# Performance work log

Measured on AMD Instinct MI355X. Metric: run time of the kernel, lower is better.

The kernel has to match this reference:

```python
import jax, jax.numpy as jnp
import numpy as np

B, S, D, H = 4, 1024, 1024, 16
DEPTH = D // H


def setup_inputs() -> dict:
    key = jax.random.key(0)
    ks = jax.random.split(key, 13)
    inp = {
        'query': jax.random.normal(ks[0], (B, S, D), dtype=jnp.float32),
        'key': jax.random.normal(ks[1], (B, S, D), dtype=jnp.float32),
        'value': jax.random.normal(ks[2], (B, S, D), dtype=jnp.float32),
        'mask': jax.random.bernoulli(ks[3], 0.1, (B, S, S)),
    }
    scale = 1.0 / np.sqrt(D)
    inp['wq_w'] = jax.random.uniform(ks[4], (D, D), jnp.float32, -scale, scale)
    inp['wq_b'] = jax.random.uniform(ks[5], (D,), jnp.float32, -scale, scale)
    inp['wk_w'] = jax.random.uniform(ks[6], (D, D), jnp.float32, -scale, scale)
    inp['wk_b'] = jax.random.uniform(ks[7], (D,), jnp.float32, -scale, scale)
    inp['wv_w'] = jax.random.uniform(ks[8], (D, D), jnp.float32, -scale, scale)
    inp['wv_b'] = jax.random.uniform(ks[9], (D,), jnp.float32, -scale, scale)
    inp['fc_w'] = jax.random.uniform(ks[10], (D, D), jnp.float32, -scale, scale)
    inp['fc_b'] = jax.random.uniform(ks[11], (D,), jnp.float32, -scale, scale)
    return inp


def _split_heads(x):
    # [B,S,D] -> [B,H,S,depth]
    b, s, _ = x.shape
    return x.reshape(b, s, H, DEPTH).transpose(0, 2, 1, 3)


def reference(query, key, value, mask, wq_w, wq_b, wk_w, wk_b, wv_w, wv_b, fc_w, fc_b):
    q = _split_heads(query @ wq_w.T + wq_b)
    k = _split_heads(key @ wk_w.T + wk_b)
    v = _split_heads(value @ wv_w.T + wv_b)
    scores = jnp.einsum('bhqd,bhkd->bhqk', q, k) / jnp.sqrt(jnp.float32(DEPTH))
    scores = jnp.where(mask[:, None, :, :], jnp.float32(-1e9), scores)
    attn = jax.nn.softmax(scores, axis=-1)
    out = jnp.einsum('bhqk,bhkd->bhqd', attn, v)  # [B,H,S,depth]
    out = out.transpose(0, 2, 1, 3).reshape(query.shape[0], -1, D)
    return out @ fc_w.T + fc_b
```

## Files before the change

kernel.cpp:

```cpp
#include <hip/hip_runtime.h>
#include <hip/hip_bf16.h>


typedef __bf16 bf16x8 __attribute__((ext_vector_type(8)));
typedef __bf16 bf16x4 __attribute__((ext_vector_type(4)));
typedef float  f32x4  __attribute__((ext_vector_type(4)));
typedef float  f32x16 __attribute__((ext_vector_type(16)));

typedef const __attribute__((address_space(1))) void* gptr_t;
typedef __attribute__((address_space(3))) void* lptr_t;

#define MFMA16(a, b, c) __builtin_amdgcn_mfma_f32_16x16x32_bf16((a), (b), (c), 0, 0, 0)
#define MFMA32(a, b, c) __builtin_amdgcn_mfma_f32_32x32x16_bf16((a), (b), (c), 0, 0, 0)

__device__ __forceinline__ void gload_lds16(const void* g, void* l) {
  __builtin_amdgcn_global_load_lds((gptr_t)g, (lptr_t)l, 16, 0, 0);
}

__device__ __forceinline__ unsigned pack2(float a, float b) {
  union { __bf16 h[2]; unsigned u; } x;
  x.h[0] = (__bf16)a; x.h[1] = (__bf16)b; return x.u;
}

__device__ __forceinline__ bf16x8 mkfrag(unsigned a, unsigned b, unsigned c, unsigned d) {
  union { unsigned w[4]; bf16x8 v; } x;
  x.w[0] = a; x.w[1] = b; x.w[2] = c; x.w[3] = d; return x.v;
}

__global__ void detect_mask(const unsigned char* m, int* flag) {
  __shared__ int s1[4], s23[4];
  int tid = threadIdx.x;
  uint4 v = ((const uint4*)m)[tid];
  unsigned x0 = v.x, x1 = v.y, x2 = v.z, x3 = v.w;
  unsigned c1  = (x0 & 0x0000ff00u) | (x1 & 0x0000ff00u) | (x2 & 0x0000ff00u) | (x3 & 0x0000ff00u);
  unsigned c23 = (x0 & 0xffff0000u) | (x1 & 0xffff0000u) | (x2 & 0xffff0000u) | (x3 & 0xffff0000u);
  unsigned long long b1 = __ballot(c1 != 0), b23 = __ballot(c23 != 0);
  if ((tid & 63) == 0) { s1[tid >> 6] = (b1 != 0); s23[tid >> 6] = (b23 != 0); }
  __syncthreads();
  if (tid == 0) {
    int a1 = s1[0] | s1[1] | s1[2] | s1[3];
    int a23 = s23[0] | s23[1] | s23[2] | s23[3];
    *flag = a1 ? 1 : (a23 ? 2 : 0);
  }
}

__global__ void pack_mask(const void* m, const int* flag, unsigned int* out) {
  size_t i = (size_t)blockIdx.x * 256 + threadIdx.x;
  int f = *flag;
  bool v;
  if (f == 1)      v = ((const unsigned char*)m)[i] != 0;
  else if (f == 2) v = ((const float*)m)[i] != 0.0f;
  else             v = ((const int*)m)[i] != 0;
  unsigned long long bal = __ballot(v);
  int lane = threadIdx.x & 63;
  if ((lane & 31) == 0) out[i >> 5] = (unsigned int)(bal >> (lane & 32));
}

__global__ void cvt_all(const float* q, const float* k, const float* v,
                        const float* w0, const float* w1, const float* w2, const float* w3,
                        __bf16* oq, __bf16* ok, __bf16* ov,
                        __bf16* o0, __bf16* o1, __bf16* o2, __bf16* o3) {
  int bid = blockIdx.x;
  const float* in; __bf16* out; int sub;
  if (bid < 12288) {
    int w = bid >> 12; sub = bid & 4095;
    in = w == 0 ? q : w == 1 ? k : v;
    out = w == 0 ? oq : w == 1 ? ok : ov;
  } else {
    int w = (bid - 12288) >> 10; sub = (bid - 12288) & 1023;
    in = w == 0 ? w0 : w == 1 ? w1 : w == 2 ? w2 : w3;
    out = w == 0 ? o0 : w == 1 ? o1 : w == 2 ? o2 : o3;
  }
  size_t i = (size_t)sub * 256 + threadIdx.x;
  float4 vv = ((const float4*)in)[i];
  bf16x4 o; o[0] = (__bf16)vv.x; o[1] = (__bf16)vv.y; o[2] = (__bf16)vv.z; o[3] = (__bf16)vv.w;
  ((bf16x4*)out)[i] = o;
}

__global__ __launch_bounds__(512, 2)
void gemm_qkv8(const __bf16* __restrict__ qb, const __bf16* __restrict__ kb,
               const __bf16* __restrict__ vb,
               const __bf16* __restrict__ wq, const __bf16* __restrict__ wk,
               const __bf16* __restrict__ wv,
               const float* __restrict__ bq, const float* __restrict__ bk,
               const float* __restrict__ bv,
               __bf16* __restrict__ Qp, __bf16* __restrict__ Kp, __bf16* __restrict__ Vt) {
  __shared__ __bf16 As[2][256 * 64];
  __shared__ __bf16 Bs[2][256 * 64];
  const int bm = blockIdx.x;
  const int bnall = blockIdx.y;
  const int which = bnall >> 2;
  const int bnl = bnall & 3;
  const __bf16* A = which == 0 ? qb : which == 1 ? kb : vb;
  const __bf16* W = which == 0 ? wq : which == 1 ? wk : wv;
  const float* bias = which == 0 ? bq : which == 1 ? bk : bv;

  const int tid = threadIdx.x, wave = tid >> 6, lane = tid & 63;
  const int wr = wave >> 2, wc = wave & 3;
  const int l15 = lane & 15, l4 = lane >> 4;
  const int srow = tid >> 3;
  const int sgw = ((tid & 7) ^ (srow & 7)) << 3;
  f32x4 acc[8][4] = {};

#define STAGE_HALF(bb, u, hp)                                                   \
  {                                                                             \
    _Pragma("unroll")                                                           \
    for (int i_ = 0; i_ < 2; ++i_) {                                            \
      int row_ = ((hp) & 1) * 128 + i_ * 64 + srow;                             \
      if ((hp) < 2)                                                             \
        gload_lds16(A + (size_t)(bm * 256 + row_) * 1024 + (u) * 64 + sgw,      \
                    &As[bb][(((hp) & 1) * 128 + i_ * 64 + wave * 8) * 64]);     \
      else                                                                      \
        gload_lds16(W + (size_t)(bnl * 256 + row_) * 1024 + (u) * 64 + sgw,     \
                    &Bs[bb][(((hp) & 1) * 128 + i_ * 64 + wave * 8) * 64]);     \
    }                                                                           \
  }

#define PHASE(curb, mh, nh, DOSTAGE)                                            \
  {                                                                             \
    bf16x8 af_[4][2], bf_[2][2];                                                \
    _Pragma("unroll")                                                           \
    for (int j_ = 0; j_ < 4; ++j_) {                                            \
      int row_ = wr * 128 + ((mh) * 4 + j_) * 16 + l15;                         \
      _Pragma("unroll")                                                         \
      for (int k_ = 0; k_ < 2; ++k_)                                            \
        af_[j_][k_] = *(const bf16x8*)(&As[curb][row_ * 64 +                    \
                          (((k_ * 4 + l4) ^ (row_ & 7)) << 3)]);                \
    }                                                                           \
    _Pragma("unroll")                                                           \
    for (int n_ = 0; n_ < 2; ++n_) {                                            \
      int row_ = wc * 64 + ((nh) * 2 + n_) * 16 + l15;                          \
      _Pragma("unroll")                                                         \
      for (int k_ = 0; k_ < 2; ++k_)                                            \
        bf_[n_][k_] = *(const bf16x8*)(&Bs[curb][row_ * 64 +                    \
                          (((k_ * 4 + l4) ^ (row_ & 7)) << 3)]);                \
    }                                                                           \
    DOSTAGE;                                                                    \
    __builtin_amdgcn_s_barrier();                                               \
    __builtin_amdgcn_sched_barrier(0);                                          \
    __builtin_amdgcn_s_setprio(1);                                              \
    _Pragma("unroll")                                                           \
    for (int k_ = 0; k_ < 2; ++k_)                                              \
      _Pragma("unroll")                                                         \
      for (int j_ = 0; j_ < 4; ++j_)                                            \
        _Pragma("unroll")                                                       \
        for (int n_ = 0; n_ < 2; ++n_)                                          \
          acc[(mh) * 4 + j_][(nh) * 2 + n_] =                                   \
              MFMA16(af_[j_][k_], bf_[n_][k_], acc[(mh) * 4 + j_][(nh) * 2 + n_]); \
    __builtin_amdgcn_s_setprio(0);                                              \
    __builtin_amdgcn_s_barrier();                                               \
    __builtin_amdgcn_sched_barrier(0);                                          \
  }

  STAGE_HALF(0, 0, 0); STAGE_HALF(0, 0, 1); STAGE_HALF(0, 0, 2); STAGE_HALF(0, 0, 3);
  int cur = 0;
#pragma unroll 1
  for (int u = 0; u < 16; ++u) {
    const int nu = u < 15 ? u + 1 : 15;
    const int oth = cur ^ 1;
    STAGE_HALF(oth, nu, 0);
    asm volatile("s_waitcnt vmcnt(2)" ::: "memory");
    __builtin_amdgcn_s_barrier();
    __builtin_amdgcn_sched_barrier(0);
    PHASE(cur, 0, 0, {});
    PHASE(cur, 1, 0, STAGE_HALF(oth, nu, 1));
    PHASE(cur, 0, 1, STAGE_HALF(oth, nu, 2));
    PHASE(cur, 1, 1, STAGE_HALF(oth, nu, 3));
    cur ^= 1;
  }

  const int r0 = l4 * 4, cl = l15;
  const float osc = (which == 0) ? 0.18033688011112042f : 1.0f;
  __bf16* Onat = which == 0 ? Qp : Kp;
#pragma unroll
  for (int ni = 0; ni < 4; ++ni) {
    int col = bnl * 256 + wc * 64 + ni * 16 + cl;
    float bvv = bias[col];
#pragma unroll
    for (int mi = 0; mi < 8; ++mi) {
      int rowb = bm * 256 + wr * 128 + mi * 16 + r0;
      if (which < 2) {
#pragma unroll
        for (int r = 0; r < 4; ++r)
          Onat[(size_t)(rowb + r) * 1024 + col] = (__bf16)((acc[mi][ni][r] + bvv) * osc);
      } else {
        int bb = rowb >> 10, s0 = rowb & 1023, hh = col >> 6, d = col & 63;
        bf16x4 ov;
#pragma unroll
        for (int r = 0; r < 4; ++r) ov[r] = (__bf16)(acc[mi][ni][r] + bvv);
        *(bf16x4*)(Vt + (((size_t)(bb * 16 + hh) * 64 + d) << 10) + s0) = ov;
      }
    }
  }
#undef STAGE_HALF
#undef PHASE
}

__global__ __launch_bounds__(256, 2)
void gemm_fc(const __bf16* __restrict__ A, const __bf16* __restrict__ W,
             const float* __restrict__ bias, float* __restrict__ C) {
  __shared__ __bf16 As[2][128 * 64];
  __shared__ __bf16 Bs[2][128 * 64];
  const int bm = blockIdx.x, bn = blockIdx.y;
  const int tid = threadIdx.x, wave = tid >> 6, lane = tid & 63;
  const int wr = wave >> 1, wc = wave & 1;
  const int rl = lane >> 3, c8 = lane & 7;
  f32x4 acc[4][4] = {};

#define FC_STAGE(bb, kt)                                                              \
  {                                                                                   \
    _Pragma("unroll")                                                                 \
    for (int i = 0; i < 4; ++i) {                                                     \
      int row = wave * 32 + i * 8 + rl;                                               \
      int sw = (c8 ^ (row & 7)) << 3;                                                 \
      gload_lds16(A + (size_t)(bm * 128 + row) * 1024 + (kt) * 64 + sw,               \
                  &As[bb][(wave * 32 + i * 8) * 64]);                                 \
      gload_lds16(W + (size_t)(bn * 128 + row) * 1024 + (kt) * 64 + sw,               \
                  &Bs[bb][(wave * 32 + i * 8) * 64]);                                 \
    }                                                                                 \
  }

  FC_STAGE(0, 0);
  __syncthreads();
  int buf = 0;
  for (int kt = 0; kt < 16; ++kt) {
    if (kt < 15) FC_STAGE(buf ^ 1, kt + 1);
#pragma unroll
    for (int k32 = 0; k32 < 2; ++k32) {
      bf16x8 af[4], bfr[4];
#pragma unroll
      for (int mi = 0; mi < 4; ++mi) {
        int row = wr * 64 + mi * 16 + (lane & 15);
        af[mi] = *(const bf16x8*)(&As[buf][row * 64 + (((k32 * 4 + (lane >> 4)) ^ (row & 7)) << 3)]);
      }
#pragma unroll
      for (int ni = 0; ni < 4; ++ni) {
        int row = wc * 64 + ni * 16 + (lane & 15);
        bfr[ni] = *(const bf16x8*)(&Bs[buf][row * 64 + (((k32 * 4 + (lane >> 4)) ^ (row & 7)) << 3)]);
      }
#pragma unroll
      for (int mi = 0; mi < 4; ++mi)
#pragma unroll
        for (int ni = 0; ni < 4; ++ni)
          acc[mi][ni] = MFMA16(af[mi], bfr[ni], acc[mi][ni]);
    }
    __syncthreads();
    buf ^= 1;
  }
  const int r0 = (lane >> 4) * 4, cl = lane & 15;
#pragma unroll
  for (int ni = 0; ni < 4; ++ni) {
    int col = bn * 128 + wc * 64 + ni * 16 + cl;
    float bvv = bias[col];
#pragma unroll
    for (int mi = 0; mi < 4; ++mi) {
      int rowb = bm * 128 + wr * 64 + mi * 16 + r0;
#pragma unroll
      for (int r = 0; r < 4; ++r)
        C[(size_t)(rowb + r) * 1024 + col] = acc[mi][ni][r] + bvv;
    }
  }
}

__global__ __launch_bounds__(256)
void attn32(const __bf16* __restrict__ Qp, const __bf16* __restrict__ Kp,
            const __bf16* __restrict__ Vt, const unsigned int* __restrict__ mp,
            __bf16* __restrict__ O) {
  __shared__ __bf16 Ks[2][64 * 64];
  __shared__ __bf16 Vs[2][64 * 64];
  const int tid = threadIdx.x, wave = tid >> 6, lane = tid & 63;
  const int lo5 = lane & 31, hi = lane >> 5;
  const int bx = blockIdx.x;
  const int qt = bx & 7, h = (bx >> 3) & 15, b = bx >> 7;
  const int qrow = qt * 128 + wave * 32 + lo5;

  const int srow = tid >> 3;
  const int sgx = ((tid & 7) ^ (srow & 7)) << 3;

#define ATTN_STAGE(bb, kt)                                                            \
  {                                                                                   \
    _Pragma("unroll")                                                                 \
    for (int i = 0; i < 2; ++i) {                                                     \
      gload_lds16(Kp + (size_t)(b * 1024 + (kt) * 64 + i * 32 + srow) * 1024          \
                     + h * 64 + sgx,                                                  \
                  &Ks[bb][i * 2048 + wave * 512]);                                    \
      gload_lds16(Vt + (size_t)((b * 16 + h) * 64 + i * 32 + srow) * 1024             \
                     + (kt) * 64 + sgx,                                               \
                  &Vs[bb][i * 2048 + wave * 512]);                                    \
    }                                                                                 \
  }

  bf16x8 qf[4];
  const __bf16* qb = Qp + ((size_t)(b * 1024 + qrow)) * 1024 + h * 64 + hi * 8;
#pragma unroll
  for (int m = 0; m < 4; ++m) qf[m] = *(const bf16x8*)(qb + m * 16);

  bf16x8 onesf;
#pragma unroll
  for (int i = 0; i < 8; ++i) onesf[i] = (__bf16)1.0f;

  f32x16 oacc0 = {}, oacc1 = {}, oaccD = {};
  const uint2* mrow = ((const uint2*)mp) + ((size_t)(b * 1024 + qrow)) * 16;
  const int x = lo5 & 7;

  ATTN_STAGE(0, 0);
  uint2 mwc = mrow[0];
  __syncthreads();
  int buf = 0;
  for (int kt = 0; kt < 16; ++kt) {
    if (kt < 15) ATTN_STAGE(buf ^ 1, kt + 1);
    uint2 mwn = mwc;
    if (kt < 15) mwn = mrow[kt + 1];
#pragma unroll
    for (int sub = 0; sub < 2; ++sub) {
      f32x16 s = {};
#pragma unroll
      for (int m = 0; m < 4; ++m) {
        bf16x8 kf = *(const bf16x8*)(&Ks[buf][(sub * 32 + lo5) * 64 + (((2 * m + hi) ^ x) << 3)]);
        s = MFMA32(kf, qf[m], s);
      }
      unsigned w32 = sub == 0 ? mwc.x : mwc.y;
      unsigned nw = ~(w32 >> (hi * 4));
      float p[16];
#pragma unroll
      for (int r = 0; r < 16; ++r) {
        float e = __builtin_amdgcn_exp2f(s[r]);
        unsigned keep = (unsigned)__builtin_amdgcn_sbfe((int)nw, (unsigned)((r & 3) + 8 * (r >> 2)), 1u);
        p[r] = __uint_as_float(__float_as_uint(e) & keep);
      }
      unsigned own[8];
#pragma unroll
      for (int u = 0; u < 4; ++u) {
        own[2 * u]     = pack2(p[4 * u],     p[4 * u + 1]);
        own[2 * u + 1] = pack2(p[4 * u + 2], p[4 * u + 3]);
      }
#pragma unroll
      for (int sf = 0; sf < 2; ++sf) {
        unsigned a0 = own[4 * sf + 0], b0 = own[4 * sf + 2];
        unsigned a1 = own[4 * sf + 1], b1 = own[4 * sf + 3];
        asm volatile("v_permlane32_swap_b32 %0, %1" : "+v"(a0), "+v"(b0));
        asm volatile("v_permlane32_swap_b32 %0, %1" : "+v"(a1), "+v"(b1));
        bf16x8 pa = mkfrag(a0, a1, b0, b1);
        int g = ((sub * 4 + sf * 2 + hi) ^ x) << 3;
        bf16x8 vf0 = *(const bf16x8*)(&Vs[buf][lo5 * 64 + g]);
        bf16x8 vf1 = *(const bf16x8*)(&Vs[buf][(lo5 + 32) * 64 + g]);
        oacc0 = MFMA32(pa, vf0, oacc0);
        oacc1 = MFMA32(pa, vf1, oacc1);
        oaccD = MFMA32(pa, onesf, oaccD);
      }
    }
    __syncthreads();
    buf ^= 1;
    mwc = mwn;
  }

  const size_t orow0 = (size_t)(b * 1024 + qt * 128 + wave * 32);
#pragma unroll
  for (int r = 0; r < 16; ++r) {
    int cr = (r & 3) + 8 * (r >> 2) + 4 * hi;
    float iv = __builtin_amdgcn_rcpf(oaccD[r]);
    __bf16* op = O + (orow0 + cr) * 1024 + h * 64 + lo5;
    op[0]  = (__bf16)(oacc0[r] * iv);
    op[32] = (__bf16)(oacc1[r] * iv);
  }
}

extern "C" void kernel_launch(void* const* d_in, const int* in_sizes, int n_in,
                              void* d_out, int out_size, void* d_ws, size_t ws_size,
                              hipStream_t stream) {
  const float* query = (const float*)d_in[0];
  const float* key   = (const float*)d_in[1];
  const float* value = (const float*)d_in[2];
  const void*  mask  = d_in[3];
  const float* wq_w  = (const float*)d_in[4];
  const float* wq_b  = (const float*)d_in[5];
  const float* wk_w  = (const float*)d_in[6];
  const float* wk_b  = (const float*)d_in[7];
  const float* wv_w  = (const float*)d_in[8];
  const float* wv_b  = (const float*)d_in[9];
  const float* fc_w  = (const float*)d_in[10];
  const float* fc_b  = (const float*)d_in[11];

  char* ws = (char*)d_ws;
  __bf16* qb  = (__bf16*)ws;
  __bf16* kb  = qb  + 4194304;
  __bf16* vb  = kb  + 4194304;
  __bf16* wqb = vb  + 4194304;
  __bf16* wkb = wqb + 1048576;
  __bf16* wvb = wkb + 1048576;
  __bf16* fcb = wvb + 1048576;
  __bf16* Qp  = fcb + 1048576;
  __bf16* Kp  = Qp  + 4194304;
  __bf16* Vt  = Kp  + 4194304;
  __bf16* Ob  = Vt  + 4194304;
  unsigned int* mpk = (unsigned int*)(Ob + 4194304);
  int* flag = (int*)(mpk + 131072);

  detect_mask<<<1, 256, 0, stream>>>((const unsigned char*)mask, flag);
  pack_mask<<<16384, 256, 0, stream>>>(mask, flag, mpk);
  cvt_all<<<16384, 256, 0, stream>>>(query, key, value, wq_w, wk_w, wv_w, fc_w,
                                     qb, kb, vb, wqb, wkb, wvb, fcb);
  dim3 g1(16, 12);
  gemm_qkv8<<<g1, 512, 0, stream>>>(qb, kb, vb, wqb, wkb, wvb, wq_b, wk_b, wv_b, Qp, Kp, Vt);
  attn32<<<512, 256, 0, stream>>>(Qp, Kp, Vt, mpk, Ob);
  dim3 g2(32, 8);
  gemm_fc<<<g2, 256, 0, stream>>>(Ob, fcb, fc_b, (float*)d_out);
}
```

Baseline: 240.7 us.

## Switch projection and output GEMMs to 32x32x16 MFMA with full-tile prefetch

Both the QKV projection GEMM and the output FC GEMM now use 32x32x16 bf16 MFMA instructions with f32x16 accumulators instead of 16x16x32, and the LDS fragment indexing and epilogue row mapping change to match. The QKV kernel stops interleaving its next-tile global-to-LDS loads across the four compute phases. It now issues all next-tile loads up front, waits with explicit vmcnt, and runs two K-half phases per tile. The FC kernel gets the same barrier and vmcnt pipeline with setprio in place of __syncthreads. The larger MFMA shape needs fewer instructions and fragment reads per FLOP, but the epilogue stores become more scattered and the loads overlap less finely with compute.

```diff
diff --git a/kernel.cpp b/kernel.cpp
--- a/kernel.cpp
+++ b/kernel.cpp
@@ -97,10 +97,10 @@
 
   const int tid = threadIdx.x, wave = tid >> 6, lane = tid & 63;
   const int wr = wave >> 2, wc = wave & 3;
-  const int l15 = lane & 15, l4 = lane >> 4;
+  const int lo5 = lane & 31, hi = lane >> 5;
   const int srow = tid >> 3;
   const int sgw = ((tid & 7) ^ (srow & 7)) << 3;
-  f32x4 acc[8][4] = {};
+  f32x16 acc[4][2] = {};
 
 #define STAGE_HALF(bb, u, hp)                                                   \
   {                                                                             \
@@ -116,37 +116,35 @@
     }                                                                           \
   }
 
-#define PHASE(curb, mh, nh, DOSTAGE)                                            \
+#define PHASEK(curb, kh)                                                        \
   {                                                                             \
     bf16x8 af_[4][2], bf_[2][2];                                                \
     _Pragma("unroll")                                                           \
-    for (int j_ = 0; j_ < 4; ++j_) {                                            \
-      int row_ = wr * 128 + ((mh) * 4 + j_) * 16 + l15;                         \
-      _Pragma("unroll")                                                         \
-      for (int k_ = 0; k_ < 2; ++k_)                                            \
-        af_[j_][k_] = *(const bf16x8*)(&As[curb][row_ * 64 +                    \
-                          (((k_ * 4 + l4) ^ (row_ & 7)) << 3)]);                \
+    for (int mi_ = 0; mi_ < 4; ++mi_) {                                         \
+      int row_ = wr * 128 + mi_ * 32 + lo5;                                     \
+      _Pragma("unroll")                                                         \
+      for (int kk_ = 0; kk_ < 2; ++kk_)                                         \
+        af_[mi_][kk_] = *(const bf16x8*)(&As[curb][row_ * 64 +                  \
+            (((((kh) * 2 + kk_) * 2 + hi) ^ (row_ & 7)) << 3)]);                \
     }                                                                           \
     _Pragma("unroll")                                                           \
-    for (int n_ = 0; n_ < 2; ++n_) {                                            \
-      int row_ = wc * 64 + ((nh) * 2 + n_) * 16 + l15;                          \
-      _Pragma("unroll")                                                         \
-      for (int k_ = 0; k_ < 2; ++k_)                                            \
-        bf_[n_][k_] = *(const bf16x8*)(&Bs[curb][row_ * 64 +                    \
-                          (((k_ * 4 + l4) ^ (row_ & 7)) << 3)]);                \
+    for (int ni_ = 0; ni_ < 2; ++ni_) {                                         \
+      int row_ = wc * 64 + ni_ * 32 + lo5;                                      \
+      _Pragma("unroll")                                                         \
+      for (int kk_ = 0; kk_ < 2; ++kk_)                                         \
+        bf_[ni_][kk_] = *(const bf16x8*)(&Bs[curb][row_ * 64 +                  \
+            (((((kh) * 2 + kk_) * 2 + hi) ^ (row_ & 7)) << 3)]);                \
     }                                                                           \
-    DOSTAGE;                                                                    \
     __builtin_amdgcn_s_barrier();                                               \
     __builtin_amdgcn_sched_barrier(0);                                          \
     __builtin_amdgcn_s_setprio(1);                                              \
     _Pragma("unroll")                                                           \
-    for (int k_ = 0; k_ < 2; ++k_)                                              \
-      _Pragma("unroll")                                                         \
-      for (int j_ = 0; j_ < 4; ++j_)                                            \
+    for (int kk_ = 0; kk_ < 2; ++kk_)                                           \
+      _Pragma("unroll")                                                         \
+      for (int mi_ = 0; mi_ < 4; ++mi_)                                         \
         _Pragma("unroll")                                                       \
-        for (int n_ = 0; n_ < 2; ++n_)                                          \
-          acc[(mh) * 4 + j_][(nh) * 2 + n_] =                                   \
-              MFMA16(af_[j_][k_], bf_[n_][k_], acc[(mh) * 4 + j_][(nh) * 2 + n_]); \
+        for (int ni_ = 0; ni_ < 2; ++ni_)                                       \
+          acc[mi_][ni_] = MFMA32(af_[mi_][kk_], bf_[ni_][kk_], acc[mi_][ni_]);  \
     __builtin_amdgcn_s_setprio(0);                                              \
     __builtin_amdgcn_s_barrier();                                               \
     __builtin_amdgcn_sched_barrier(0);                                          \
@@ -156,44 +154,52 @@
   int cur = 0;
 #pragma unroll 1
   for (int u = 0; u < 16; ++u) {
-    const int nu = u < 15 ? u + 1 : 15;
     const int oth = cur ^ 1;
-    STAGE_HALF(oth, nu, 0);
-    asm volatile("s_waitcnt vmcnt(2)" ::: "memory");
+    if (u < 15) {
+      STAGE_HALF(oth, u + 1, 0); STAGE_HALF(oth, u + 1, 1);
+      STAGE_HALF(oth, u + 1, 2); STAGE_HALF(oth, u + 1, 3);
+      asm volatile("s_waitcnt vmcnt(8)" ::: "memory");
+    } else {
+      asm volatile("s_waitcnt vmcnt(0)" ::: "memory");
+    }
     __builtin_amdgcn_s_barrier();
     __builtin_amdgcn_sched_barrier(0);
-    PHASE(cur, 0, 0, {});
-    PHASE(cur, 1, 0, STAGE_HALF(oth, nu, 1));
-    PHASE(cur, 0, 1, STAGE_HALF(oth, nu, 2));
-    PHASE(cur, 1, 1, STAGE_HALF(oth, nu, 3));
+    PHASEK(cur, 0);
+    PHASEK(cur, 1);
     cur ^= 1;
   }
 
-  const int r0 = l4 * 4, cl = l15;
   const float osc = (which == 0) ? 0.18033688011112042f : 1.0f;
   __bf16* Onat = which == 0 ? Qp : Kp;
 #pragma unroll
-  for (int ni = 0; ni < 4; ++ni) {
-    int col = bnl * 256 + wc * 64 + ni * 16 + cl;
-    float bvv = bias[col];
-#pragma unroll
-    for (int mi = 0; mi < 8; ++mi) {
-      int rowb = bm * 256 + wr * 128 + mi * 16 + r0;
+  for (int mi = 0; mi < 4; ++mi) {
+    int rowb0 = bm * 256 + wr * 128 + mi * 32;
+#pragma unroll
+    for (int ni = 0; ni < 2; ++ni) {
+      int col = bnl * 256 + wc * 64 + ni * 32 + lo5;
+      float bvv = bias[col];
       if (which < 2) {
 #pragma unroll
-        for (int r = 0; r < 4; ++r)
-          Onat[(size_t)(rowb + r) * 1024 + col] = (__bf16)((acc[mi][ni][r] + bvv) * osc);
+        for (int r = 0; r < 16; ++r) {
+          int rw = rowb0 + (r & 3) + 8 * (r >> 2) + 4 * hi;
+          Onat[(size_t)rw * 1024 + col] = (__bf16)((acc[mi][ni][r] + bvv) * osc);
+        }
       } else {
-        int bb = rowb >> 10, s0 = rowb & 1023, hh = col >> 6, d = col & 63;
-        bf16x4 ov;
-#pragma unroll
-        for (int r = 0; r < 4; ++r) ov[r] = (__bf16)(acc[mi][ni][r] + bvv);
-        *(bf16x4*)(Vt + (((size_t)(bb * 16 + hh) * 64 + d) << 10) + s0) = ov;
+        int hh = col >> 6, d = col & 63;
+        int bb2 = rowb0 >> 10;
+#pragma unroll
+        for (int q = 0; q < 4; ++q) {
+          int s0 = (rowb0 & 1023) + 8 * q + 4 * hi;
+          bf16x4 ov;
+#pragma unroll
+          for (int r = 0; r < 4; ++r) ov[r] = (__bf16)(acc[mi][ni][4 * q + r] + bvv);
+          *(bf16x4*)(Vt + (((size_t)(bb2 * 16 + hh) * 64 + d) << 10) + s0) = ov;
+        }
       }
     }
   }
 #undef STAGE_HALF
-#undef PHASE
+#undef PHASEK
 }
 
 __global__ __launch_bounds__(256, 2)
@@ -204,8 +210,9 @@
   const int bm = blockIdx.x, bn = blockIdx.y;
   const int tid = threadIdx.x, wave = tid >> 6, lane = tid & 63;
   const int wr = wave >> 1, wc = wave & 1;
+  const int lo5 = lane & 31, hi = lane >> 5;
   const int rl = lane >> 3, c8 = lane & 7;
-  f32x4 acc[4][4] = {};
+  f32x16 acc[2][2] = {};
 
 #define FC_STAGE(bb, kt)                                                              \
   {                                                                                   \
@@ -220,46 +227,74 @@
     }                                                                                 \
   }
 
+#define FPHASEK(curb, kh)                                                       \
+  {                                                                             \
+    bf16x8 af_[2][2], bf_[2][2];                                                \
+    _Pragma("unroll")                                                           \
+    for (int mi_ = 0; mi_ < 2; ++mi_) {                                         \
+      int row_ = wr * 64 + mi_ * 32 + lo5;                                      \
+      _Pragma("unroll")                                                         \
+      for (int kk_ = 0; kk_ < 2; ++kk_)                                         \
+        af_[mi_][kk_] = *(const bf16x8*)(&As[curb][row_ * 64 +                  \
+            (((((kh) * 2 + kk_) * 2 + hi) ^ (row_ & 7)) << 3)]);                \
+    }                                                                           \
+    _Pragma("unroll")                                                           \
+    for (int ni_ = 0; ni_ < 2; ++ni_) {                                         \
+      int row_ = wc * 64 + ni_ * 32 + lo5;                                      \
+      _Pragma("unroll")                                                         \
+      for (int kk_ = 0; kk_ < 2; ++kk_)                                         \
+        bf_[ni_][kk_] = *(const bf16x8*)(&Bs[curb][row_ * 64 +                  \
+            (((((kh) * 2 + kk_) * 2 + hi) ^ (row_ & 7)) << 3)]);                \
+    }                                                                           \
+    __builtin_amdgcn_s_barrier();                                               \
+    __builtin_amdgcn_sched_barrier(0);                                          \
+    __builtin_amdgcn_s_setprio(1);                                              \
+    _Pragma("unroll")                                                           \
+    for (int kk_ = 0; kk_ < 2; ++kk_)                                           \
+      _Pragma("unroll")                                                         \
+      for (int mi_ = 0; mi_ < 2; ++mi_)                                         \
+        _Pragma("unroll")                                                       \
+        for (int ni_ = 0; ni_ < 2; ++ni_)                                       \
+          acc[mi_][ni_] = MFMA32(af_[mi_][kk_], bf_[ni_][kk_], acc[mi_][ni_]);  \
+    __builtin_amdgcn_s_setprio(0);                                              \
+    __builtin_amdgcn_s_barrier();                                               \
+    __builtin_amdgcn_sched_barrier(0);                                          \
+  }
+
   FC_STAGE(0, 0);
-  __syncthreads();
   int buf = 0;
+#pragma unroll 1
   for (int kt = 0; kt < 16; ++kt) {
-    if (kt < 15) FC_STAGE(buf ^ 1, kt + 1);
-#pragma unroll
-    for (int k32 = 0; k32 < 2; ++k32) {
-      bf16x8 af[4], bfr[4];
-#pragma unroll
-      for (int mi = 0; mi < 4; ++mi) {
-        int row = wr * 64 + mi * 16 + (lane & 15);
-        af[mi] = *(const bf16x8*)(&As[buf][row * 64 + (((k32 * 4 + (lane >> 4)) ^ (row & 7)) << 3)]);
-      }
-#pragma unroll
-      for (int ni = 0; ni < 4; ++ni) {
-        int row = wc * 64 + ni * 16 + (lane & 15);
-        bfr[ni] = *(const bf16x8*)(&Bs[buf][row * 64 + (((k32 * 4 + (lane >> 4)) ^ (row & 7)) << 3)]);
-      }
-#pragma unroll
-      for (int mi = 0; mi < 4; ++mi)
-#pragma unroll
-        for (int ni = 0; ni < 4; ++ni)
-          acc[mi][ni] = MFMA16(af[mi], bfr[ni], acc[mi][ni]);
+    if (kt < 15) {
+      FC_STAGE(buf ^ 1, kt + 1);
+      asm volatile("s_waitcnt vmcnt(8)" ::: "memory");
+    } else {
+      asm volatile("s_waitcnt vmcnt(0)" ::: "memory");
     }
-    __syncthreads();
+    __builtin_amdgcn_s_barrier();
+    __builtin_amdgcn_sched_barrier(0);
+    FPHASEK(buf, 0);
+    FPHASEK(buf, 1);
     buf ^= 1;
   }
-  const int r0 = (lane >> 4) * 4, cl = lane & 15;
-#pragma unroll
-  for (int ni = 0; ni < 4; ++ni) {
-    int col = bn * 128 + wc * 64 + ni * 16 + cl;
-    float bvv = bias[col];
-#pragma unroll
-    for (int mi = 0; mi < 4; ++mi) {
-      int rowb = bm * 128 + wr * 64 + mi * 16 + r0;
-#pragma unroll
-      for (int r = 0; r < 4; ++r)
-        C[(size_t)(rowb + r) * 1024 + col] = acc[mi][ni][r] + bvv;
+
+  const float* __restrict__ bp = bias;
+#pragma unroll
+  for (int mi = 0; mi < 2; ++mi) {
+    int rowb0 = bm * 128 + wr * 64 + mi * 32;
+#pragma unroll
+    for (int ni = 0; ni < 2; ++ni) {
+      int col = bn * 128 + wc * 64 + ni * 32 + lo5;
+      float bvv = bp[col];
+#pragma unroll
+      for (int r = 0; r < 16; ++r) {
+        int rw = rowb0 + (r & 3) + 8 * (r >> 2) + 4 * hi;
+        C[(size_t)rw * 1024 + col] = acc[mi][ni][r] + bvv;
+      }
     }
   }
+#undef FC_STAGE
+#undef FPHASEK
 }
 
 __global__ __launch_bounds__(256)
```

Measured after the change: 244.5 us. No clear change (+1.6%).
